# Kernel optimization log

Measured on AMD Instinct MI355X. Metric: run time of the kernel, lower is better.

## Reference

```python
import jax, jax.numpy as jnp
import numpy as np

N, E, IN, H, ED = 50000, 800000, 128, 128, 3
EPS = 1e-5

def _gat_conv(x, src, dst, ea, W, a_src, a_dst, We, a_edge, bias):
    n = x.shape[0]
    # add self loops; self-loop edge_attr = per-feature mean (PyG fill_value='mean')
    loops = jnp.arange(n, dtype=src.dtype)
    s = jnp.concatenate([src, loops])
    d = jnp.concatenate([dst, loops])
    ea_full = jnp.concatenate([ea, jnp.broadcast_to(ea.mean(0), (n, ea.shape[1]))], 0)
    h = x @ W                       # [n, H]
    al_s = h @ a_src                # [n]
    al_d = h @ a_dst
    al_e = (ea_full @ We) @ a_edge  # [E+n]
    alpha = jax.nn.leaky_relu(al_s[s] + al_d[d] + al_e, 0.2)
    # segment softmax over destination nodes (every node has a self loop)
    amax = jax.ops.segment_max(alpha, d, num_segments=n)
    ex = jnp.exp(alpha - amax[d])
    denom = jax.ops.segment_sum(ex, d, num_segments=n)
    coef = ex / (denom[d] + 1e-16)
    out = jax.ops.segment_sum(h[s] * coef[:, None], d, num_segments=n)
    return out + bias

def _bn(x, gamma, beta):
    mu = x.mean(0)
    var = ((x - mu) ** 2).mean(0)
    return (x - mu) * jax.lax.rsqrt(var + EPS) * gamma + beta

def setup_inputs():
    key = jax.random.key(0)
    ks = jax.random.split(key, 40)
    inp = {
        "x": jax.random.normal(ks[0], (N, IN), jnp.float32),
        "edge_index": jax.random.randint(ks[1], (2, E), 0, N, dtype=jnp.int32),
        "batch": jnp.zeros((N,), jnp.int32),
        "edge_attr": jax.random.normal(ks[2], (E, ED), jnp.float32),
    }
    i = 3
    for l, cin in ((1, IN), (2, H), (3, H)):
        s = 1.0 / np.sqrt(cin)
        inp[f"W{l}"] = jax.random.normal(ks[i], (cin, H), jnp.float32) * s; i += 1
        inp[f"as{l}"] = jax.random.normal(ks[i], (H,), jnp.float32) * 0.1; i += 1
        inp[f"ad{l}"] = jax.random.normal(ks[i], (H,), jnp.float32) * 0.1; i += 1
        inp[f"We{l}"] = jax.random.normal(ks[i], (ED, H), jnp.float32) * 0.5; i += 1
        inp[f"ae{l}"] = jax.random.normal(ks[i], (H,), jnp.float32) * 0.1; i += 1
        inp[f"b{l}"] = jnp.zeros((H,), jnp.float32)
        inp[f"g{l}"] = jnp.ones((H,), jnp.float32)
        inp[f"be{l}"] = jnp.zeros((H,), jnp.float32)
    return inp

def reference(x, edge_index, batch, edge_attr,
              W1, as1, ad1, We1, ae1, b1, g1, be1,
              W2, as2, ad2, We2, ae2, b2, g2, be2,
              W3, as3, ad3, We3, ae3, b3, g3, be3):
    src, dst = edge_index[0], edge_index[1]
    h = _gat_conv(x, src, dst, edge_attr, W1, as1, ad1, We1, ae1, b1)
    h = _bn(jax.nn.leaky_relu(h, 0.01), g1, be1)
    h = _gat_conv(h, src, dst, edge_attr, W2, as2, ad2, We2, ae2, b2)
    h = _bn(jax.nn.leaky_relu(h, 0.01), g2, be2)
    h = _gat_conv(h, src, dst, edge_attr, W3, as3, ad3, We3, ae3, b3)
    h = _bn(jax.nn.leaky_relu(h, 0.01), g3, be3)
    return h
```

## Files before the change

### kernel.cpp

```cpp
#include <hip/hip_runtime.h>
#include <hip/hip_fp16.h>
#include <math.h>


#define NB 64

struct __align__(16) Edge2 { int src; int dst; unsigned e01; unsigned e2; };

__device__ __forceinline__ unsigned short f2bf(float x) {
  unsigned u = __float_as_uint(x);
  unsigned r = (u + 0x7FFFu + ((u >> 16) & 1u)) >> 16;
  return (unsigned short)r;
}
__device__ __forceinline__ float bf_lo(unsigned u) { return __uint_as_float(u << 16); }
__device__ __forceinline__ float bf_hi(unsigned u) { return __uint_as_float(u & 0xFFFF0000u); }

__global__ void k_hist_lds(const int* __restrict__ dst, const float* __restrict__ ea, int E,
                           int n, unsigned* __restrict__ hist32, float* __restrict__ ea_sum) {
  extern __shared__ unsigned cnt[];
  int nh = (n + 1) >> 1;
  for (int i = threadIdx.x; i < nh; i += blockDim.x) cnt[i] = 0u;
  __syncthreads();
  int tid = blockIdx.x * blockDim.x + threadIdx.x;
  int stride = gridDim.x * blockDim.x;
  float s0 = 0.f, s1 = 0.f, s2 = 0.f;
  for (int i = tid; i < E; i += stride) {
    int d = dst[i];
    atomicAdd(&cnt[d >> 1], 1u << ((d & 1) << 4));
    s0 += ea[i * 3 + 0]; s1 += ea[i * 3 + 1]; s2 += ea[i * 3 + 2];
  }
  for (int off = 32; off; off >>= 1) {
    s0 += __shfl_down(s0, off); s1 += __shfl_down(s1, off); s2 += __shfl_down(s2, off);
  }
  if ((threadIdx.x & 63) == 0) {
    atomicAdd(&ea_sum[0], s0); atomicAdd(&ea_sum[1], s1); atomicAdd(&ea_sum[2], s2);
  }
  __syncthreads();
  unsigned* plane = hist32 + (size_t)blockIdx.x * nh;
  for (int i = threadIdx.x; i < nh; i += blockDim.x) plane[i] = cnt[i];
}

__device__ __forceinline__ int wave_incl_scan(int x, int lane) {
  for (int off = 1; off < 64; off <<= 1) {
    int t = __shfl_up(x, off);
    if (lane >= off) x += t;
  }
  return x;
}

__global__ __launch_bounds__(1024) void k_scan_a(const unsigned* __restrict__ hist32, int n,
                                                 int* __restrict__ start,
                                                 int* __restrict__ bsum) {
  __shared__ int wsum[16];
  int t = threadIdx.x, lane = t & 63, w = t >> 6;
  int i = blockIdx.x * 1024 + t;
  int nh = (n + 1) >> 1;
  int stride2 = nh * 2;
  const unsigned short* h16 = (const unsigned short*)hist32;
  int v = 0;
  if (i < n) {
    for (int r = 0; r < NB; ++r) v += h16[(size_t)r * stride2 + i];
  }
  int x = wave_incl_scan(v, lane);
  if (lane == 63) wsum[w] = x;
  __syncthreads();
  if (w == 0 && lane < 16) {
    int s = wsum[lane];
    for (int off = 1; off < 16; off <<= 1) {
      int u = __shfl_up(s, off);
      if (lane >= off) s += u;
    }
    wsum[lane] = s;
  }
  __syncthreads();
  int woff = w ? wsum[w - 1] : 0;
  if (i < n) start[i] = x - v + woff;
  if (t == 1023) bsum[blockIdx.x] = wsum[15];
}

__global__ void k_scan_b(int* __restrict__ bsum, int nb, int* __restrict__ start, int n) {
  int lane = threadIdx.x;
  int v = (lane < nb) ? bsum[lane] : 0;
  int x = wave_incl_scan(v, lane);
  if (lane < nb) bsum[lane] = x - v;
  if (lane == nb - 1) start[n] = x;
}

__global__ void k_scan_c(int* __restrict__ start, const int* __restrict__ bsum,
                         const unsigned* __restrict__ hist32, int n,
                         int* __restrict__ cursorp) {
  int i = blockIdx.x * blockDim.x + threadIdx.x;
  if (i >= n) return;
  int nh = (n + 1) >> 1;
  int stride2 = nh * 2;
  const unsigned short* h16 = (const unsigned short*)hist32;
  int s = start[i] + bsum[i >> 10];
  start[i] = s;
  int run = s;
  for (int r = 0; r < NB; ++r) {
    cursorp[(size_t)r * n + i] = run;
    run += h16[(size_t)r * stride2 + i];
  }
}

__global__ void k_scatter_lds(const int* __restrict__ src, const int* __restrict__ dst,
                              const float* __restrict__ ea, int E, int n,
                              const int* __restrict__ cursorp, Edge2* __restrict__ edges) {
  extern __shared__ unsigned cnt[];
  int nh = (n + 1) >> 1;
  for (int i = threadIdx.x; i < nh; i += blockDim.x) cnt[i] = 0u;
  __syncthreads();
  const int* cur = cursorp + (size_t)blockIdx.x * n;
  int tid = blockIdx.x * blockDim.x + threadIdx.x;
  int stride = gridDim.x * blockDim.x;
  for (int i = tid; i < E; i += stride) {
    int d = dst[i];
    int sh = (d & 1) << 4;
    unsigned old = atomicAdd(&cnt[d >> 1], 1u << sh);
    int rank = (old >> sh) & 0xFFFF;
    int pos = cur[d] + rank;
    unsigned short h0 = __half_as_ushort(__float2half(ea[i * 3 + 0]));
    unsigned short h1 = __half_as_ushort(__float2half(ea[i * 3 + 1]));
    unsigned short h2 = __half_as_ushort(__float2half(ea[i * 3 + 2]));
    Edge2 e;
    e.src = src[i];
    e.dst = d;
    e.e01 = (unsigned)h0 | ((unsigned)h1 << 16);
    e.e2 = (unsigned)h2;
    edges[pos] = e;
  }
}

__device__ __forceinline__ void param_wave(const float* __restrict__ We,
                                           const float* __restrict__ ae,
                                           const float* __restrict__ ea_sum, float invE,
                                           float* __restrict__ P, int lane) {
  float a0 = ae[lane], a1 = ae[64 + lane];
  float p0 = We[0 * 128 + lane] * a0 + We[0 * 128 + 64 + lane] * a1;
  float p1 = We[1 * 128 + lane] * a0 + We[1 * 128 + 64 + lane] * a1;
  float p2 = We[2 * 128 + lane] * a0 + We[2 * 128 + 64 + lane] * a1;
  for (int off = 32; off; off >>= 1) {
    p0 += __shfl_down(p0, off); p1 += __shfl_down(p1, off); p2 += __shfl_down(p2, off);
  }
  if (lane == 0) {
    P[0] = p0; P[1] = p1; P[2] = p2;
    P[3] = ea_sum[0] * invE * p0 + ea_sum[1] * invE * p1 + ea_sum[2] * invE * p2;
  }
}

__global__ void k_param0(const float* __restrict__ We, const float* __restrict__ ae,
                         const float* __restrict__ ea_sum, float invE, float* __restrict__ P,
                         float* __restrict__ scale, float* __restrict__ shift,
                         float* __restrict__ colstats) {
  int t = threadIdx.x;
  if (t < 64) {
    param_wave(We, ae, ea_sum, invE, P, t);
  } else if (t < 192) {
    int c = t - 64;
    scale[c] = 1.f; shift[c] = 0.f;
    colstats[c] = 0.f; colstats[128 + c] = 0.f;
  }
}

__global__ void k_inter(const float* __restrict__ colstatsIn, const float* __restrict__ g,
                        const float* __restrict__ be, float invN,
                        float* __restrict__ scale, float* __restrict__ shift,
                        const float* __restrict__ WeN, const float* __restrict__ aeN,
                        const float* __restrict__ ea_sum, float invE, float* __restrict__ P,
                        float* __restrict__ colstats) {
  int t = threadIdx.x;
  if (t < 64) {
    param_wave(WeN, aeN, ea_sum, invE, P, t);
  } else if (t < 192) {
    int c = t - 64;
    float mu = colstatsIn[c] * invN;
    float var = colstatsIn[128 + c] * invN - mu * mu;
    var = var > 0.f ? var : 0.f;
    float sc = g[c] * rsqrtf(var + 1e-5f);
    scale[c] = sc;
    shift[c] = be[c] - mu * sc;
    colstats[c] = 0.f; colstats[128 + c] = 0.f;
  }
}

__global__ __launch_bounds__(256) void k_gemm2(
    const float* __restrict__ X, const float* __restrict__ Wm,
    const float* __restrict__ bnsc, const float* __restrict__ bnsh,
    const float* __restrict__ as, const float* __restrict__ ad,
    const float* __restrict__ P,
    unsigned* __restrict__ hb, float* __restrict__ al_s, float* __restrict__ al_d,
    float* __restrict__ es, int n) {
  __shared__ float wl[128 * 128];
  __shared__ float xs[32 * 128];
  int t = threadIdx.x;
  for (int i = t; i < 4096; i += 256) ((float4*)wl)[i] = ((const float4*)Wm)[i];
  int c32 = t & 31;
  int c4 = c32 << 2;
  int rq = t >> 5;
  int lane = t & 63;
  float4 av_s = *(const float4*)(as + c4);
  float4 av_d = *(const float4*)(ad + c4);
  float cself = P[3];
  int ntiles = (n + 31) >> 5;
  for (int tile = blockIdx.x; tile < ntiles; tile += gridDim.x) {
    int r0 = tile << 5;
    __syncthreads();
    for (int i = t; i < 1024; i += 256) {
      int rr = i >> 5, cc = i & 31;
      int g = r0 + rr;
      float4 v;
      if (g < n) {
        v = ((const float4*)(X + (size_t)g * 128))[cc];
        float4 sc = ((const float4*)bnsc)[cc];
        float4 sh = ((const float4*)bnsh)[cc];
        v.x = fmaf(v.x, sc.x, sh.x); v.y = fmaf(v.y, sc.y, sh.y);
        v.z = fmaf(v.z, sc.z, sh.z); v.w = fmaf(v.w, sc.w, sh.w);
      } else { v.x = v.y = v.z = v.w = 0.f; }
      ((float4*)xs)[i] = v;
    }
    __syncthreads();
    float4 acc[4];
    for (int r = 0; r < 4; ++r) { acc[r].x = acc[r].y = acc[r].z = acc[r].w = 0.f; }
    const float* xr = xs + (rq << 2) * 128;
#pragma unroll 4
    for (int k = 0; k < 128; ++k) {
      float4 w4 = ((const float4*)wl)[(k << 5) + c32];
#pragma unroll
      for (int r = 0; r < 4; ++r) {
        float xv = xr[r * 128 + k];
        acc[r].x = fmaf(xv, w4.x, acc[r].x);
        acc[r].y = fmaf(xv, w4.y, acc[r].y);
        acc[r].z = fmaf(xv, w4.z, acc[r].z);
        acc[r].w = fmaf(xv, w4.w, acc[r].w);
      }
    }
    int gbase = r0 + (rq << 2);
#pragma unroll
    for (int r = 0; r < 4; ++r) {
      int g = gbase + r;
      float4 o = acc[r];
      if (g < n) {
        unsigned u01 = ((unsigned)f2bf(o.y) << 16) | (unsigned)f2bf(o.x);
        unsigned u23 = ((unsigned)f2bf(o.w) << 16) | (unsigned)f2bf(o.z);
        uint2 uu = {u01, u23};
        *(uint2*)(hb + (size_t)g * 64 + (c32 << 1)) = uu;
      }
      float ps = o.x * av_s.x + o.y * av_s.y + o.z * av_s.z + o.w * av_s.w;
      float pd = o.x * av_d.x + o.y * av_d.y + o.z * av_d.z + o.w * av_d.w;
      for (int off = 16; off; off >>= 1) {
        ps += __shfl_xor(ps, off);
        pd += __shfl_xor(pd, off);
      }
      if ((lane & 31) == 0 && g < n) {
        al_s[g] = ps; al_d[g] = pd;
        float a = ps + pd + cself;
        a = a > 0.f ? a : 0.2f * a;
        es[g] = __expf(a);
      }
    }
  }
}

__global__ __launch_bounds__(256) void k_alpha3(const int4* __restrict__ edges,
                                                const float* __restrict__ al_s,
                                                const float* __restrict__ al_d,
                                                const float* __restrict__ P,
                                                int2* __restrict__ meta, int E) {
  int i = blockIdx.x * blockDim.x + threadIdx.x;
  if (i >= E) return;
  int4 ev = edges[i];
  float e0 = __half2float(__ushort_as_half((unsigned short)(ev.z & 0xFFFF)));
  float e1 = __half2float(__ushort_as_half((unsigned short)(((unsigned)ev.z) >> 16)));
  float e2 = __half2float(__ushort_as_half((unsigned short)(ev.w & 0xFFFF)));
  float a = al_s[ev.x] + al_d[ev.y] + e0 * P[0] + e1 * P[1] + e2 * P[2];
  a = a > 0.f ? a : 0.2f * a;
  int2 mv;
  mv.x = ev.x;
  mv.y = __float_as_int(__expf(a));
  meta[i] = mv;
}

__global__ __launch_bounds__(256) void k_agg5(const int2* __restrict__ meta,
                                              const int* __restrict__ start,
                                              const unsigned* __restrict__ hb,
                                              const float* __restrict__ es,
                                              const float* __restrict__ bias,
                                              float* __restrict__ y,
                                              float* __restrict__ colsum,
                                              float* __restrict__ colsumsq, int n) {
  int lane = threadIdx.x & 63;
  int w = threadIdx.x >> 6;
  int gw = (blockIdx.x * blockDim.x + threadIdx.x) >> 6;
  int nw = (gridDim.x * blockDim.x) >> 6;
  float2 b2 = ((const float2*)bias)[lane];
  float s0 = 0.f, s1 = 0.f, q0 = 0.f, q1 = 0.f;
  for (int i = gw; i < n; i += nw) {
    int e0 = __builtin_amdgcn_readfirstlane(start[i]);
    int e1 = __builtin_amdgcn_readfirstlane(start[i + 1]);
    float eself = es[i];
    unsigned hv = hb[(size_t)i * 64 + lane];
    float aX0 = eself * bf_lo(hv), aY0 = eself * bf_hi(hv);
    float aX1 = 0.f, aY1 = 0.f, aX2 = 0.f, aY2 = 0.f, aX3 = 0.f, aY3 = 0.f;
    float pacc = 0.f;
    for (int base = e0; base < e1; base += 64) {
      int m = e1 - base;
      if (m > 64) m = 64;
      int2 mv;
      mv.x = 0; mv.y = 0;
      if (lane < m) mv = meta[base + lane];
      float t = (lane < m) ? __int_as_float(mv.y) : 0.f;
      for (int off = 32; off; off >>= 1) t += __shfl_xor(t, off);
      pacc += t;
      int k = 0;
      for (; k + 8 <= m; k += 8) {
        unsigned gv[8];
        float pv[8];
#pragma unroll
        for (int j = 0; j < 8; ++j) {
          int ssv = __builtin_amdgcn_readlane(mv.x, k + j);
          pv[j] = __uint_as_float((unsigned)__builtin_amdgcn_readlane(mv.y, k + j));
          gv[j] = hb[(size_t)ssv * 64 + lane];
        }
#pragma unroll
        for (int j = 0; j < 8; ++j) {
          float gx = bf_lo(gv[j]);
          float gy = bf_hi(gv[j]);
          if ((j & 3) == 0) { aX0 = fmaf(pv[j], gx, aX0); aY0 = fmaf(pv[j], gy, aY0); }
          else if ((j & 3) == 1) { aX1 = fmaf(pv[j], gx, aX1); aY1 = fmaf(pv[j], gy, aY1); }
          else if ((j & 3) == 2) { aX2 = fmaf(pv[j], gx, aX2); aY2 = fmaf(pv[j], gy, aY2); }
          else { aX3 = fmaf(pv[j], gx, aX3); aY3 = fmaf(pv[j], gy, aY3); }
        }
      }
      for (; k < m; ++k) {
        int ssv = __builtin_amdgcn_readlane(mv.x, k);
        float pv = __uint_as_float((unsigned)__builtin_amdgcn_readlane(mv.y, k));
        unsigned gvv = hb[(size_t)ssv * 64 + lane];
        aX0 = fmaf(pv, bf_lo(gvv), aX0);
        aY0 = fmaf(pv, bf_hi(gvv), aY0);
      }
    }
    float inv = 1.0f / (eself + pacc + 1e-16f);
    float o0 = (aX0 + aX1) + (aX2 + aX3);
    float o1 = (aY0 + aY1) + (aY2 + aY3);
    o0 = fmaf(o0, inv, b2.x);
    o1 = fmaf(o1, inv, b2.y);
    o0 = o0 > 0.f ? o0 : 0.01f * o0;
    o1 = o1 > 0.f ? o1 : 0.01f * o1;
    float2 o2 = {o0, o1};
    ((float2*)(y + (size_t)i * 128))[lane] = o2;
    s0 += o0; s1 += o1;
    q0 = fmaf(o0, o0, q0); q1 = fmaf(o1, o1, q1);
  }
  __shared__ float red[4][4][64];
  red[0][w][lane] = s0; red[1][w][lane] = s1; red[2][w][lane] = q0; red[3][w][lane] = q1;
  __syncthreads();
  if (w == 0) {
    for (int ww = 1; ww < 4; ++ww) {
      s0 += red[0][ww][lane]; s1 += red[1][ww][lane];
      q0 += red[2][ww][lane]; q1 += red[3][ww][lane];
    }
    atomicAdd(&colsum[2 * lane], s0);
    atomicAdd(&colsum[2 * lane + 1], s1);
    atomicAdd(&colsumsq[2 * lane], q0);
    atomicAdd(&colsumsq[2 * lane + 1], q1);
  }
}

__global__ __launch_bounds__(256) void k_bnapply_final(
    const float4* __restrict__ yin, const float* __restrict__ colstats,
    const float* __restrict__ g, const float* __restrict__ be, float invN,
    float4* __restrict__ yout, int total4) {
  __shared__ float sc_s[128], sh_s[128];
  int t = threadIdx.x;
  if (t < 128) {
    float mu = colstats[t] * invN;
    float var = colstats[128 + t] * invN - mu * mu;
    var = var > 0.f ? var : 0.f;
    float sc = g[t] * rsqrtf(var + 1e-5f);
    sc_s[t] = sc;
    sh_s[t] = be[t] - mu * sc;
  }
  __syncthreads();
  for (int i = blockIdx.x * blockDim.x + t; i < total4; i += gridDim.x * blockDim.x) {
    int c4 = (i & 31) << 2;
    float4 v = yin[i];
    v.x = fmaf(v.x, sc_s[c4 + 0], sh_s[c4 + 0]);
    v.y = fmaf(v.y, sc_s[c4 + 1], sh_s[c4 + 1]);
    v.z = fmaf(v.z, sc_s[c4 + 2], sh_s[c4 + 2]);
    v.w = fmaf(v.w, sc_s[c4 + 3], sh_s[c4 + 3]);
    yout[i] = v;
  }
}

extern "C" void kernel_launch(void* const* d_in, const int* in_sizes, int n_in,
                              void* d_out, int out_size, void* d_ws, size_t ws_size,
                              hipStream_t stream) {
  const float* x = (const float*)d_in[0];
  const int* eidx = (const int*)d_in[1];
  const float* ea = (const float*)d_in[3];
  const int H = 128;
  const int N = in_sizes[0] / H;
  const int E = in_sizes[1] / 2;
  const int* srcIdx = eidx;
  const int* dstIdx = eidx + E;
  const int nh = (N + 1) >> 1;

  char* ws = (char*)d_ws;
  size_t off = 0;
  auto alloc = [&](size_t bytes) -> void* {
    void* p = ws + off;
    off = (off + bytes + 255) & ~(size_t)255;
    return p;
  };
  Edge2* edges = (Edge2*)alloc((size_t)E * sizeof(Edge2));
  int2* meta = (int2*)alloc((size_t)E * sizeof(int2));
  unsigned* hb = (unsigned*)alloc((size_t)N * 64 * sizeof(unsigned));
  float* y = (float*)alloc((size_t)N * H * sizeof(float));
  float* al_s = (float*)alloc((size_t)N * sizeof(float));
  float* al_d = (float*)alloc((size_t)N * sizeof(float));
  float* es = (float*)alloc((size_t)N * sizeof(float));
  unsigned* hist32 = (unsigned*)alloc((size_t)NB * nh * sizeof(unsigned));
  int* cursorp = (int*)alloc((size_t)NB * N * sizeof(int));
  int* start = (int*)alloc((size_t)(N + 1) * sizeof(int));
  int* bsum = (int*)alloc(64 * sizeof(int));
  float* colstats = (float*)alloc(256 * sizeof(float));
  float* colsum = colstats;
  float* colsumsq = colstats + 128;
  float* scale = (float*)alloc(128 * sizeof(float));
  float* shift = (float*)alloc(128 * sizeof(float));
  float* ea_sum = (float*)alloc(64 * sizeof(float));
  float* P = (float*)alloc(16 * sizeof(float));

  const int nb = (N + 1023) / 1024;
  const float invE = 1.0f / (float)E;
  const float invN = 1.0f / (float)N;
  const size_t ldsBytes = (size_t)nh * sizeof(unsigned);

  hipMemsetAsync(ea_sum, 0, 64 * sizeof(float), stream);
  k_hist_lds<<<NB, 256, ldsBytes, stream>>>(dstIdx, ea, E, N, hist32, ea_sum);
  k_scan_a<<<nb, 1024, 0, stream>>>(hist32, N, start, bsum);
  k_scan_b<<<1, 64, 0, stream>>>(bsum, nb, start, N);
  k_scan_c<<<(N + 255) / 256, 256, 0, stream>>>(start, bsum, hist32, N, cursorp);
  k_scatter_lds<<<NB, 256, ldsBytes, stream>>>(srcIdx, dstIdx, ea, E, N, cursorp, edges);

  const float* Wl[3]; const float* asl[3]; const float* adl[3]; const float* Wel[3];
  const float* ael[3]; const float* bl[3]; const float* gl[3]; const float* bel[3];
  for (int l = 0; l < 3; ++l) {
    Wl[l] = (const float*)d_in[4 + 8 * l + 0];
    asl[l] = (const float*)d_in[4 + 8 * l + 1];
    adl[l] = (const float*)d_in[4 + 8 * l + 2];
    Wel[l] = (const float*)d_in[4 + 8 * l + 3];
    ael[l] = (const float*)d_in[4 + 8 * l + 4];
    bl[l] = (const float*)d_in[4 + 8 * l + 5];
    gl[l] = (const float*)d_in[4 + 8 * l + 6];
    bel[l] = (const float*)d_in[4 + 8 * l + 7];
  }

  k_param0<<<1, 192, 0, stream>>>(Wel[0], ael[0], ea_sum, invE, P, scale, shift, colstats);

  const float* X = x;
  for (int l = 0; l < 3; ++l) {
    k_gemm2<<<512, 256, 0, stream>>>(X, Wl[l], scale, shift, asl[l], adl[l], P,
                                     hb, al_s, al_d, es, N);
    k_alpha3<<<(E + 255) / 256, 256, 0, stream>>>((const int4*)edges, al_s, al_d, P,
                                                  meta, E);
    k_agg5<<<2048, 256, 0, stream>>>(meta, start, hb, es, bl[l], y,
                                     colsum, colsumsq, N);
    if (l < 2) {
      k_inter<<<1, 192, 0, stream>>>(colstats, gl[l], bel[l], invN, scale, shift,
                                     Wel[l + 1], ael[l + 1], ea_sum, invE, P, colstats);
    }
    X = y;
  }
  k_bnapply_final<<<384, 256, 0, stream>>>((const float4*)y, colstats, gl[2], bel[2], invN,
                                           (float4*)d_out, N * 32);
}
```

Before: 776.7 us.

## Split wavefront into four 16-lane groups gathering different edges with 16-byte loads

The aggregation kernel now splits each 64-lane wavefront into four groups of 16 lanes. Each group handles a different edge and loads a full 256-byte bf16 row with uint4 (16-byte) loads, instead of all 64 lanes reading 4 bytes of the same row. Every lane reads the edge metadata directly rather than using readlane broadcasts. The partial sums are then combined with cross-group shuffles, and the output column mapping and atomics are permuted to match. This aims to raise the number of gathers in flight and use wider memory transactions, at the cost of redundant metadata loads, a shuffle reduction per node, and wasted lanes when a node's edge count is not a multiple of four.

```diff
diff --git a/kernel.cpp b/kernel.cpp
--- a/kernel.cpp
+++ b/kernel.cpp
@@ -280,7 +280,7 @@
   meta[i] = mv;
 }
 
-__global__ __launch_bounds__(256) void k_agg5(const int2* __restrict__ meta,
+__global__ __launch_bounds__(256) void k_agg9(const int2* __restrict__ meta,
                                               const int* __restrict__ start,
                                               const unsigned* __restrict__ hb,
                                               const float* __restrict__ es,
@@ -290,67 +290,77 @@
                                               float* __restrict__ colsumsq, int n) {
   int lane = threadIdx.x & 63;
   int w = threadIdx.x >> 6;
+  int grp = lane >> 4;
+  int sub = lane & 15;
   int gw = (blockIdx.x * blockDim.x + threadIdx.x) >> 6;
   int nw = (gridDim.x * blockDim.x) >> 6;
-  float2 b2 = ((const float2*)bias)[lane];
+  int c0 = (sub << 3) + (grp << 1);
+  float2 b2 = ((const float2*)bias)[(sub << 2) + grp];
   float s0 = 0.f, s1 = 0.f, q0 = 0.f, q1 = 0.f;
+
+#define DO_QUAD(EB)                                                          \
+  {                                                                          \
+    int i0 = (EB), i1 = (EB) + 1, i2 = (EB) + 2, i3 = (EB) + 3;              \
+    int2 m0 = meta[i0 < e1 ? i0 : e0];                                       \
+    int2 m1 = meta[i1 < e1 ? i1 : e0];                                       \
+    int2 m2 = meta[i2 < e1 ? i2 : e0];                                       \
+    int2 m3 = meta[i3 < e1 ? i3 : e0];                                       \
+    int r0 = i0 < e1 ? m0.x : i;                                             \
+    int r1 = i1 < e1 ? m1.x : i;                                             \
+    int r2 = i2 < e1 ? m2.x : i;                                             \
+    int r3 = i3 < e1 ? m3.x : i;                                             \
+    float p0 = i0 < e1 ? __int_as_float(m0.y) : 0.f;                         \
+    float p1 = i1 < e1 ? __int_as_float(m1.y) : 0.f;                         \
+    float p2 = i2 < e1 ? __int_as_float(m2.y) : 0.f;                         \
+    float p3 = i3 < e1 ? __int_as_float(m3.y) : 0.f;                         \
+    int rr = grp == 0 ? r0 : grp == 1 ? r1 : grp == 2 ? r2 : r3;             \
+    float pp = grp == 0 ? p0 : grp == 1 ? p1 : grp == 2 ? p2 : p3;           \
+    uint4 gv = *(const uint4*)(hb + (size_t)rr * 64 + (sub << 2));           \
+    pacc += (p0 + p1) + (p2 + p3);                                           \
+    aL0 = fmaf(pp, bf_lo(gv.x), aL0); aH0 = fmaf(pp, bf_hi(gv.x), aH0);      \
+    aL1 = fmaf(pp, bf_lo(gv.y), aL1); aH1 = fmaf(pp, bf_hi(gv.y), aH1);      \
+    aL2 = fmaf(pp, bf_lo(gv.z), aL2); aH2 = fmaf(pp, bf_hi(gv.z), aH2);      \
+    aL3 = fmaf(pp, bf_lo(gv.w), aL3); aH3 = fmaf(pp, bf_hi(gv.w), aH3);      \
+  }
+
   for (int i = gw; i < n; i += nw) {
     int e0 = __builtin_amdgcn_readfirstlane(start[i]);
     int e1 = __builtin_amdgcn_readfirstlane(start[i + 1]);
     float eself = es[i];
-    unsigned hv = hb[(size_t)i * 64 + lane];
-    float aX0 = eself * bf_lo(hv), aY0 = eself * bf_hi(hv);
-    float aX1 = 0.f, aY1 = 0.f, aX2 = 0.f, aY2 = 0.f, aX3 = 0.f, aY3 = 0.f;
+    uint4 hv = *(const uint4*)(hb + (size_t)i * 64 + (sub << 2));
+    float wself = (grp == 0) ? eself : 0.f;
+    float aL0 = wself * bf_lo(hv.x), aH0 = wself * bf_hi(hv.x);
+    float aL1 = wself * bf_lo(hv.y), aH1 = wself * bf_hi(hv.y);
+    float aL2 = wself * bf_lo(hv.z), aH2 = wself * bf_hi(hv.z);
+    float aL3 = wself * bf_lo(hv.w), aH3 = wself * bf_hi(hv.w);
     float pacc = 0.f;
-    for (int base = e0; base < e1; base += 64) {
-      int m = e1 - base;
-      if (m > 64) m = 64;
-      int2 mv;
-      mv.x = 0; mv.y = 0;
-      if (lane < m) mv = meta[base + lane];
-      float t = (lane < m) ? __int_as_float(mv.y) : 0.f;
-      for (int off = 32; off; off >>= 1) t += __shfl_xor(t, off);
-      pacc += t;
-      int k = 0;
-      for (; k + 8 <= m; k += 8) {
-        unsigned gv[8];
-        float pv[8];
-#pragma unroll
-        for (int j = 0; j < 8; ++j) {
-          int ssv = __builtin_amdgcn_readlane(mv.x, k + j);
-          pv[j] = __uint_as_float((unsigned)__builtin_amdgcn_readlane(mv.y, k + j));
-          gv[j] = hb[(size_t)ssv * 64 + lane];
-        }
-#pragma unroll
-        for (int j = 0; j < 8; ++j) {
-          float gx = bf_lo(gv[j]);
-          float gy = bf_hi(gv[j]);
-          if ((j & 3) == 0) { aX0 = fmaf(pv[j], gx, aX0); aY0 = fmaf(pv[j], gy, aY0); }
-          else if ((j & 3) == 1) { aX1 = fmaf(pv[j], gx, aX1); aY1 = fmaf(pv[j], gy, aY1); }
-          else if ((j & 3) == 2) { aX2 = fmaf(pv[j], gx, aX2); aY2 = fmaf(pv[j], gy, aY2); }
-          else { aX3 = fmaf(pv[j], gx, aX3); aY3 = fmaf(pv[j], gy, aY3); }
-        }
-      }
-      for (; k < m; ++k) {
-        int ssv = __builtin_amdgcn_readlane(mv.x, k);
-        float pv = __uint_as_float((unsigned)__builtin_amdgcn_readlane(mv.y, k));
-        unsigned gvv = hb[(size_t)ssv * 64 + lane];
-        aX0 = fmaf(pv, bf_lo(gvv), aX0);
-        aY0 = fmaf(pv, bf_hi(gvv), aY0);
-      }
-    }
+    int e = e0;
+    for (; e + 8 <= e1; e += 8) {
+      DO_QUAD(e);
+      DO_QUAD(e + 4);
+    }
+    for (; e < e1; e += 4) DO_QUAD(e);
+    aL0 += __shfl_xor(aL0, 16); aL0 += __shfl_xor(aL0, 32);
+    aH0 += __shfl_xor(aH0, 16); aH0 += __shfl_xor(aH0, 32);
+    aL1 += __shfl_xor(aL1, 16); aL1 += __shfl_xor(aL1, 32);
+    aH1 += __shfl_xor(aH1, 16); aH1 += __shfl_xor(aH1, 32);
+    aL2 += __shfl_xor(aL2, 16); aL2 += __shfl_xor(aL2, 32);
+    aH2 += __shfl_xor(aH2, 16); aH2 += __shfl_xor(aH2, 32);
+    aL3 += __shfl_xor(aL3, 16); aL3 += __shfl_xor(aL3, 32);
+    aH3 += __shfl_xor(aH3, 16); aH3 += __shfl_xor(aH3, 32);
     float inv = 1.0f / (eself + pacc + 1e-16f);
-    float o0 = (aX0 + aX1) + (aX2 + aX3);
-    float o1 = (aY0 + aY1) + (aY2 + aY3);
+    float o0 = grp == 0 ? aL0 : grp == 1 ? aL1 : grp == 2 ? aL2 : aL3;
+    float o1 = grp == 0 ? aH0 : grp == 1 ? aH1 : grp == 2 ? aH2 : aH3;
     o0 = fmaf(o0, inv, b2.x);
     o1 = fmaf(o1, inv, b2.y);
     o0 = o0 > 0.f ? o0 : 0.01f * o0;
     o1 = o1 > 0.f ? o1 : 0.01f * o1;
     float2 o2 = {o0, o1};
-    ((float2*)(y + (size_t)i * 128))[lane] = o2;
+    *(float2*)(y + (size_t)i * 128 + c0) = o2;
     s0 += o0; s1 += o1;
     q0 = fmaf(o0, o0, q0); q1 = fmaf(o1, o1, q1);
   }
+#undef DO_QUAD
   __shared__ float red[4][4][64];
   red[0][w][lane] = s0; red[1][w][lane] = s1; red[2][w][lane] = q0; red[3][w][lane] = q1;
   __syncthreads();
@@ -359,10 +369,10 @@
       s0 += red[0][ww][lane]; s1 += red[1][ww][lane];
       q0 += red[2][ww][lane]; q1 += red[3][ww][lane];
     }
-    atomicAdd(&colsum[2 * lane], s0);
-    atomicAdd(&colsum[2 * lane + 1], s1);
-    atomicAdd(&colsumsq[2 * lane], q0);
-    atomicAdd(&colsumsq[2 * lane + 1], q1);
+    atomicAdd(&colsum[c0], s0);
+    atomicAdd(&colsum[c0 + 1], s1);
+    atomicAdd(&colsumsq[c0], q0);
+    atomicAdd(&colsumsq[c0 + 1], q1);
   }
 }
 
@@ -464,7 +474,7 @@
                                      hb, al_s, al_d, es, N);
     k_alpha3<<<(E + 255) / 256, 256, 0, stream>>>((const int4*)edges, al_s, al_d, P,
                                                   meta, E);
-    k_agg5<<<2048, 256, 0, stream>>>(meta, start, hb, es, bl[l], y,
+    k_agg9<<<2048, 256, 0, stream>>>(meta, start, hb, es, bl[l], y,
                                      colsum, colsumsq, N);
     if (l < 2) {
       k_inter<<<1, 192, 0, stream>>>(colstats, gl[l], bel[l], invN, scale, shift,
```

Measured after the change: 751.1 us. -3.3%, faster.
